# Kernel optimization log

Hardware: AMD Instinct MI355X
Metric: run time of the kernel (lower is better)

The kernel has to match this reference:

```python
import jax, jax.numpy as jnp
import numpy as np

THETA = 10000.0


def rope_apply(x, pos, theta=THETA):
    # x: [..., S, d] with d even; rotates interleaved pairs (2k, 2k+1),
    # matching the block-diag 2x2 rotation matmul in the torch RoPE.
    d = x.shape[-1]
    half = d // 2
    inv_freq = 1.0 / (theta ** (2.0 * jnp.arange(half, dtype=jnp.float32) / d))
    ang = pos.astype(jnp.float32)[:, None] * inv_freq[None, :]  # [S, half]
    cos, sin = jnp.cos(ang), jnp.sin(ang)
    xe, xo = x[..., 0::2], x[..., 1::2]
    oe = cos * xe - sin * xo
    oo = sin * xe + cos * xo
    return jnp.stack([oe, oo], axis=-1).reshape(x.shape)


def setup_inputs() -> dict:
    key = jax.random.key(0)
    ks = jax.random.split(key, 5)
    B, S, D = 2, 2048, 1024
    scale = 0.02
    return {
        "x": jax.random.normal(ks[0], (B, S, D), dtype=jnp.float32),
        "token_positions": jnp.arange(S, dtype=jnp.int64 if jax.config.jax_enable_x64 else jnp.int32),
        "wq": jax.random.normal(ks[1], (D, D), dtype=jnp.float32) * scale,
        "wk": jax.random.normal(ks[2], (D, D), dtype=jnp.float32) * scale,
        "wv": jax.random.normal(ks[3], (D, D), dtype=jnp.float32) * scale,
        "wo": jax.random.normal(ks[4], (D, D), dtype=jnp.float32) * scale,
    }


def reference(x, token_positions, wq, wk, wv, wo):
    B, S, D = x.shape
    H = 16
    dk = D // H

    def split_heads(t):  # [B,S,D] -> [B,H,S,dk]
        return t.reshape(B, S, H, dk).swapaxes(1, 2)

    q = split_heads(jnp.einsum('bsd,ed->bse', x, wq))
    k = split_heads(jnp.einsum('bsd,ed->bse', x, wk))
    v = split_heads(jnp.einsum('bsd,ed->bse', x, wv))

    q = rope_apply(q, token_positions)
    k = rope_apply(k, token_positions)

    scores = jnp.einsum('bhqd,bhkd->bhqk', q, k) / jnp.sqrt(jnp.float32(dk))
    causal = jnp.tril(jnp.ones((S, S), dtype=bool))
    scores = jnp.where(causal, scores, -jnp.inf)
    p = jax.nn.softmax(scores, axis=-1)
    o = jnp.einsum('bhqk,bhkd->bhqd', p, v)          # [B,H,S,dk]
    o = o.swapaxes(1, 2).reshape(B, S, D)            # merge heads
    return jnp.einsum('bse,de->bsd', o, wo)          # out proj (wo.T)
```

## Files before the change

kernel.cpp:

```cpp
#include <hip/hip_runtime.h>

typedef unsigned short u16;
typedef __attribute__((ext_vector_type(8))) short short8;
typedef __attribute__((ext_vector_type(4))) float f32x4;

__device__ __forceinline__ u16 f2b(float f) {
  union { float f; unsigned u; } v; v.f = f;
  unsigned u = v.u;
  return (u16)((u + 0x7FFFu + ((u >> 16) & 1u)) >> 16);
}
__device__ __forceinline__ u16 f2b_trunc(float f) {
  union { float f; unsigned u; } v; v.f = f;
  return (u16)(v.u >> 16);
}
__device__ __forceinline__ void glds16(const u16* g, u16* l) {
  __builtin_amdgcn_global_load_lds((const __attribute__((address_space(1))) void*)g,
                                   (__attribute__((address_space(3))) void*)l, 16, 0, 0);
}

__global__ __launch_bounds__(256) void prep_k(const float* __restrict__ x,
                                              const float* __restrict__ wq,
                                              const float* __restrict__ wk,
                                              const float* __restrict__ wv,
                                              const float* __restrict__ wo,
                                              const int* __restrict__ pos,
                                              u16* __restrict__ xb,
                                              u16* __restrict__ wqkvb,
                                              u16* __restrict__ wob,
                                              float* __restrict__ cs) {
  int bx = blockIdx.x, tid = threadIdx.x;
  if (bx < 8192) {
    const float* src; u16* dst; int base;
    if (bx < 4096)      { src = x;  dst = xb;                base = bx; }
    else if (bx < 5120) { src = wq; dst = wqkvb;             base = bx - 4096; }
    else if (bx < 6144) { src = wk; dst = wqkvb + (1 << 20); base = bx - 5120; }
    else if (bx < 7168) { src = wv; dst = wqkvb + (2 << 20); base = bx - 6144; }
    else                { src = wo; dst = wob;               base = bx - 7168; }
    int i4 = base * 1024 + tid * 4;
    const float4 v = *(const float4*)(src + i4);
    uint2 o;
    o.x = (unsigned)f2b(v.x) | ((unsigned)f2b(v.y) << 16);
    o.y = (unsigned)f2b(v.z) | ((unsigned)f2b(v.w) << 16);
    *(uint2*)(dst + i4) = o;
  } else {
    int idx = (bx - 8192) * 256 + tid;
    int i = idx & 31, s = idx >> 5;
    float p = (float)pos[s];
    float inv = expf(-(float)i * (logf(10000.0f) / 32.0f));
    float ang = p * inv;
    cs[idx * 2]     = cosf(ang);
    cs[idx * 2 + 1] = sinf(ang);
  }
}

__global__ __launch_bounds__(256, 3) void gemm_qkv(const u16* __restrict__ A,
                                                   const u16* __restrict__ B,
                                                   const float* __restrict__ cs,
                                                   u16* __restrict__ Qr,
                                                   u16* __restrict__ Kr,
                                                   u16* __restrict__ VTg) {
  const int K = 1024;
  __shared__ u16 As[128 * 64];
  __shared__ u16 Bs[128 * 64];
  const int tid = threadIdx.x;
  const int lane = tid & 63;
  const int wvid = tid >> 6;
  const int wr = wvid >> 1, wc = wvid & 1;
  const int quad = lane >> 4, l16 = lane & 15;
  const int lin = blockIdx.x + blockIdx.y * 24;
  const int chunk = lin >> 3;
  const int ncol = (lin & 7) * 3 + (chunk % 3);
  const int nrow = chunk / 3;
  const int m0 = nrow * 128, n0 = ncol * 128;
  const int sw = l16 & 7;

  f32x4 acc[4][4];
  for (int i = 0; i < 4; i++)
    for (int j = 0; j < 4; j++) acc[i][j] = (f32x4){0.f, 0.f, 0.f, 0.f};

  for (int kt = 0; kt < K; kt += 64) {
    __syncthreads();
#pragma unroll
    for (int p = 0; p < 4; p++) {
      int c = p * 256 + tid;
      int row = c >> 3, k8 = (c & 7) ^ (row & 7);
      glds16(A + (size_t)(m0 + row) * K + kt + k8 * 8, As + (size_t)(c & ~63) * 8);
    }
#pragma unroll
    for (int p = 0; p < 4; p++) {
      int c = p * 256 + tid;
      int row = c >> 3, k8 = (c & 7) ^ (row & 7);
      glds16(B + (size_t)(n0 + row) * K + kt + k8 * 8, Bs + (size_t)(c & ~63) * 8);
    }
    __syncthreads();
#pragma unroll
    for (int half = 0; half < 2; half++) {
      short8 af[4], bfr[4];
      const int kc = ((half * 4 + quad) ^ sw) * 8;
#pragma unroll
      for (int i = 0; i < 4; i++)
        af[i] = *(const short8*)(As + (wr * 64 + i * 16 + l16) * 64 + kc);
#pragma unroll
      for (int j = 0; j < 4; j++)
        bfr[j] = *(const short8*)(Bs + (wc * 64 + j * 16 + l16) * 64 + kc);
#pragma unroll
      for (int i = 0; i < 4; i++)
#pragma unroll
        for (int j = 0; j < 4; j++)
          acc[i][j] = __builtin_amdgcn_mfma_f32_16x16x32_bf16(af[i], bfr[j], acc[i][j], 0, 0, 0);
    }
  }

  const int region = n0 >> 10;
  const int b = m0 >> 11;
  if (region < 2) {
    u16* dst = region ? Kr : Qr;
    const float qs = region ? 1.0f : 0.125f * 1.44269504f;
    const bool evn = (l16 & 1) == 0;
    for (int i = 0; i < 4; i++)
      for (int j = 0; j < 4; j++) {
        int col = n0 + wc * 64 + j * 16 + l16;
        int cq = col & 1023;
        int h = cq >> 6, d = cq & 63, ifr = (d >> 1) & 31;
        for (int r = 0; r < 4; r++) {
          int s = (m0 & 2047) + wr * 64 + i * 16 + quad * 4 + r;
          float v = acc[i][j][r];
          float vp = __shfl_xor(v, 1);
          if (evn) {
            float2 c2 = *(const float2*)(cs + (s * 32 + ifr) * 2);
            float oe = (c2.x * v - c2.y * vp) * qs;
            float oo = (c2.y * v + c2.x * vp) * qs;
            unsigned pk = (unsigned)f2b(oe) | ((unsigned)f2b(oo) << 16);
            *(unsigned*)(dst + ((size_t)(b * 16 + h) * 2048 + s) * 64 + d) = pk;
          }
        }
      }
  } else {
    for (int j = 0; j < 4; j++) {
      int col = n0 + wc * 64 + j * 16 + l16;
      int cq = col & 1023;
      int h = cq >> 6, d = cq & 63;
      u16* base = VTg + ((size_t)(b * 16 + h) * 64 + d) * 2048;
      for (int i = 0; i < 4; i++) {
        int s0 = (m0 & 2047) + wr * 64 + i * 16 + quad * 4;
        uint2 o;
        o.x = (unsigned)f2b(acc[i][j][0]) | ((unsigned)f2b(acc[i][j][1]) << 16);
        o.y = (unsigned)f2b(acc[i][j][2]) | ((unsigned)f2b(acc[i][j][3]) << 16);
        *(uint2*)(base + s0) = o;
      }
    }
  }
}

__global__ __launch_bounds__(256, 2) void gemm_bt_f32(const u16* __restrict__ A,
                                                      const u16* __restrict__ B,
                                                      float* __restrict__ C,
                                                      int M, int N, int K) {
  __shared__ u16 As[64 * 64];
  __shared__ u16 Bs[128 * 64];
  const int tid = threadIdx.x;
  const int wv = tid >> 6, lane = tid & 63;
  const int quad = lane >> 4, l16 = lane & 15;
  const int m0 = blockIdx.y * 64, n0 = blockIdx.x * 128;
  const int sw = l16 & 7;

  f32x4 acc[4][2];
  for (int i = 0; i < 4; i++)
    for (int j = 0; j < 2; j++) acc[i][j] = (f32x4){0.f, 0.f, 0.f, 0.f};

  for (int kt = 0; kt < K; kt += 64) {
    __syncthreads();
#pragma unroll
    for (int p = 0; p < 2; p++) {
      int c = p * 256 + tid;
      int row = c >> 3, k8 = (c & 7) ^ (row & 7);
      glds16(A + (size_t)(m0 + row) * K + kt + k8 * 8, As + (size_t)(c & ~63) * 8);
    }
#pragma unroll
    for (int p = 0; p < 4; p++) {
      int c = p * 256 + tid;
      int row = c >> 3, k8 = (c & 7) ^ (row & 7);
      glds16(B + (size_t)(n0 + row) * K + kt + k8 * 8, Bs + (size_t)(c & ~63) * 8);
    }
    __syncthreads();
#pragma unroll
    for (int half = 0; half < 2; half++) {
      short8 af[4], bfr[2];
      const int kc = ((half * 4 + quad) ^ sw) * 8;
#pragma unroll
      for (int i = 0; i < 4; i++)
        af[i] = *(const short8*)(As + (i * 16 + l16) * 64 + kc);
#pragma unroll
      for (int j = 0; j < 2; j++)
        bfr[j] = *(const short8*)(Bs + (wv * 32 + j * 16 + l16) * 64 + kc);
#pragma unroll
      for (int i = 0; i < 4; i++)
#pragma unroll
        for (int j = 0; j < 2; j++)
          acc[i][j] = __builtin_amdgcn_mfma_f32_16x16x32_bf16(af[i], bfr[j], acc[i][j], 0, 0, 0);
    }
  }
  for (int i = 0; i < 4; i++)
    for (int j = 0; j < 2; j++) {
      int col = n0 + wv * 32 + j * 16 + l16;
      for (int r = 0; r < 4; r++) {
        int row = m0 + i * 16 + quad * 4 + r;
        C[(size_t)row * N + col] = acc[i][j][r];
      }
    }
}

struct AttnSM {
  u16 Ks[2][8 * 512];
  u16 Vt[2][8 * 512];
  u16 Ps[2][8 * 520];
};

template <bool DIAG>
__device__ __forceinline__ void attn_tile(const u16* Ksb, const u16* Vtb, u16* Psb,
                                          short8 qa0, short8 qa1, f32x4* oacc,
                                          f32x4& lacc, int wl, int quad, int l16) {
  const int rowbase = wl * 16 + quad * 4;
#pragma unroll
  for (int nt = 0; nt < 4; nt++) {
    f32x4 s4 = (f32x4){0.f, 0.f, 0.f, 0.f};
    short8 b0 = *(const short8*)(Ksb + quad * 512 + (nt * 16 + l16) * 8);
    short8 b1 = *(const short8*)(Ksb + (4 + quad) * 512 + (nt * 16 + l16) * 8);
    s4 = __builtin_amdgcn_mfma_f32_16x16x32_bf16(qa0, b0, s4, 0, 0, 0);
    s4 = __builtin_amdgcn_mfma_f32_16x16x32_bf16(qa1, b1, s4, 0, 0, 0);
    int col = nt * 16 + l16;
    int cp = col >> 3, co = col & 7;
#pragma unroll
    for (int r = 0; r < 4; r++) {
      float v = s4[r];
      if (DIAG && col > rowbase + r) v = -1e30f;
      float p = exp2f(v);
      int row = rowbase + r;
      int A = (cp + 2 * (row >> 3)) & 7;
      Psb[A * 520 + row * 8 + co] = f2b_trunc(p);
    }
  }
  int mr = wl * 16 + l16;
  int A0 = (quad + 2 * (mr >> 3)) & 7;
  short8 pa0 = *(const short8*)(Psb + A0 * 520 + mr * 8);
  short8 pa1 = *(const short8*)(Psb + ((A0 + 4) & 7) * 520 + mr * 8);
  const short8 ones = (short8){(short)0x3F80, (short)0x3F80, (short)0x3F80, (short)0x3F80,
                               (short)0x3F80, (short)0x3F80, (short)0x3F80, (short)0x3F80};
  lacc = __builtin_amdgcn_mfma_f32_16x16x32_bf16(pa0, ones, lacc, 0, 0, 0);
  lacc = __builtin_amdgcn_mfma_f32_16x16x32_bf16(pa1, ones, lacc, 0, 0, 0);
  int sl0 = quad ^ (l16 & 7);
#pragma unroll
  for (int nt = 0; nt < 4; nt++) {
    int d = nt * 16 + l16;
    short8 vb0 = *(const short8*)(Vtb + d * 64 + sl0 * 8);
    short8 vb1 = *(const short8*)(Vtb + d * 64 + (sl0 ^ 4) * 8);
    oacc[nt] = __builtin_amdgcn_mfma_f32_16x16x32_bf16(pa0, vb0, oacc[nt], 0, 0, 0);
    oacc[nt] = __builtin_amdgcn_mfma_f32_16x16x32_bf16(pa1, vb1, oacc[nt], 0, 0, 0);
  }
}

__global__ __launch_bounds__(512, 4) void attn_k(const u16* __restrict__ Q,
                                                 const u16* __restrict__ K,
                                                 const u16* __restrict__ VT,
                                                 u16* __restrict__ O, int S) {
  __shared__ AttnSM sm;
  const int tid = threadIdx.x;
  const int wv = tid >> 6, lane = tid & 63, quad = lane >> 4, l16 = lane & 15;
  const int grp = wv >> 2, wl = wv & 3;
  const int bh = blockIdx.x, slot = blockIdx.y;
  const int qtB = 31 - slot;
  const int qtMy = grp ? qtB : slot;
  const int q0My = qtMy * 64;
  const u16* Qg = Q + (size_t)bh * S * 64;
  const u16* Kg = K + (size_t)bh * S * 64;
  const u16* Vg = VT + (size_t)bh * S * 64;
  const int vrow_off = lane >> 3;
  const int vchunk = (lane & 7) ^ (lane >> 3);

  const u16* qrow = Qg + (size_t)(q0My + wl * 16 + l16) * 64;
  short8 qa0 = *(const short8*)(qrow + quad * 8);
  short8 qa1 = *(const short8*)(qrow + 32 + quad * 8);

  f32x4 oacc[4];
  for (int j = 0; j < 4; j++) oacc[j] = (f32x4){0.f, 0.f, 0.f, 0.f};
  f32x4 lacc = (f32x4){0.f, 0.f, 0.f, 0.f};
  u16* Psb = &sm.Ps[grp][0];

  glds16(Kg + (size_t)lane * 64 + wv * 8, &sm.Ks[0][wv * 512]);
  glds16(Vg + (size_t)(wv * 8 + vrow_off) * S + vchunk * 8, &sm.Vt[0][wv * 512]);

  for (int kt = 0; kt <= qtB; kt++) {
    const int cur = kt & 1;
    __syncthreads();
    if (kt < qtB) {
      const int kn = (kt + 1) * 64;
      glds16(Kg + (size_t)(kn + lane) * 64 + wv * 8, &sm.Ks[cur ^ 1][wv * 512]);
      glds16(Vg + (size_t)(wv * 8 + vrow_off) * S + kn + vchunk * 8, &sm.Vt[cur ^ 1][wv * 512]);
    }
    if (kt < qtMy)
      attn_tile<false>(&sm.Ks[cur][0], &sm.Vt[cur][0], Psb, qa0, qa1, oacc, lacc, wl, quad, l16);
    else if (kt == qtMy)
      attn_tile<true>(&sm.Ks[cur][0], &sm.Vt[cur][0], Psb, qa0, qa1, oacc, lacc, wl, quad, l16);
  }

  const int b = bh >> 4, h = bh & 15;
  const bool evn = (l16 & 1) == 0;
  const int rowbase = wl * 16 + quad * 4;
  float l_inv[4];
#pragma unroll
  for (int r = 0; r < 4; r++) l_inv[r] = 1.f / lacc[r];
#pragma unroll
  for (int nt = 0; nt < 4; nt++) {
    int col = nt * 16 + l16;
#pragma unroll
    for (int r = 0; r < 4; r++) {
      float v = oacc[nt][r] * l_inv[r];
      float vp = __shfl_xor(v, 1);
      if (evn) {
        int s = q0My + rowbase + r;
        unsigned pk = (unsigned)f2b(v) | ((unsigned)f2b(vp) << 16);
        *(unsigned*)(O + ((size_t)(b * S + s) * 16 + h) * 64 + col) = pk;
      }
    }
  }
}

extern "C" void kernel_launch(void* const* d_in, const int* in_sizes, int n_in,
                              void* d_out, int out_size, void* d_ws, size_t ws_size,
                              hipStream_t stream) {
  const float* x  = (const float*)d_in[0];
  const int*   tp = (const int*)d_in[1];
  const float* wq = (const float*)d_in[2];
  const float* wk = (const float*)d_in[3];
  const float* wvp = (const float*)d_in[4];
  const float* wo = (const float*)d_in[5];
  float* out = (float*)d_out;

  const int S = 2048, D = 1024;
  const int BS = 2 * S;

  char* ws = (char*)d_ws;
  u16*   xb    = (u16*)(ws);
  u16*   wqkvb = (u16*)(ws + ((size_t)8 << 20));
  u16*   wob   = (u16*)(ws + ((size_t)14 << 20));
  float* cs    = (float*)(ws + ((size_t)16 << 20));
  u16*   qr    = (u16*)(ws + ((size_t)17 << 20));
  u16*   kr    = (u16*)(ws + ((size_t)25 << 20));
  u16*   vtg   = (u16*)(ws + ((size_t)33 << 20));
  u16*   ob    = (u16*)(ws + ((size_t)42 << 20));

  prep_k<<<8448, 256, 0, stream>>>(x, wq, wk, wvp, wo, tp, xb, wqkvb, wob, cs);

  dim3 g1(3 * D / 128, BS / 128);
  gemm_qkv<<<g1, 256, 0, stream>>>(xb, wqkvb, cs, qr, kr, vtg);

  dim3 ga(32, 16);
  attn_k<<<ga, 512, 0, stream>>>(qr, kr, vtg, ob, S);

  dim3 g2(D / 128, BS / 64);
  gemm_bt_f32<<<g2, 256, 0, stream>>>(ob, wob, out, BS, D, D);
}
```

Baseline: 179.0 us.

## Process both paired query tiles per wave to share K/V fragment loads

The attention kernel drops from 512 to 256 threads per block, and each wave now handles rows from both the low and the high query tile of a causal pair. A new fused tile routine reuses each K and V LDS fragment for the two query tiles, where before two wave groups each loaded them separately. It also removes the idle time of the first group, which previously sat out the iterations past its diagonal. In exchange each thread holds twice the accumulators, raising register pressure, and there are fewer waves per block to hide latency.

```diff
diff --git a/kernel.cpp b/kernel.cpp
--- a/kernel.cpp
+++ b/kernel.cpp
@@ -259,35 +259,102 @@
   }
 }
 
-__global__ __launch_bounds__(512, 4) void attn_k(const u16* __restrict__ Q,
+template <bool DIAGA>
+__device__ __forceinline__ void attn_tile2(const u16* Ksb, const u16* Vtb,
+                                           u16* PsA, u16* PsB,
+                                           short8 qaA0, short8 qaA1,
+                                           short8 qaB0, short8 qaB1,
+                                           f32x4* oaccA, f32x4* oaccB,
+                                           f32x4& laccA, f32x4& laccB,
+                                           int wl, int quad, int l16) {
+  const int rowbase = wl * 16 + quad * 4;
+#pragma unroll
+  for (int nt = 0; nt < 4; nt++) {
+    short8 b0 = *(const short8*)(Ksb + quad * 512 + (nt * 16 + l16) * 8);
+    short8 b1 = *(const short8*)(Ksb + (4 + quad) * 512 + (nt * 16 + l16) * 8);
+    f32x4 sA = (f32x4){0.f, 0.f, 0.f, 0.f};
+    f32x4 sB = (f32x4){0.f, 0.f, 0.f, 0.f};
+    sA = __builtin_amdgcn_mfma_f32_16x16x32_bf16(qaA0, b0, sA, 0, 0, 0);
+    sA = __builtin_amdgcn_mfma_f32_16x16x32_bf16(qaA1, b1, sA, 0, 0, 0);
+    sB = __builtin_amdgcn_mfma_f32_16x16x32_bf16(qaB0, b0, sB, 0, 0, 0);
+    sB = __builtin_amdgcn_mfma_f32_16x16x32_bf16(qaB1, b1, sB, 0, 0, 0);
+    int col = nt * 16 + l16;
+    int cp = col >> 3, co = col & 7;
+#pragma unroll
+    for (int r = 0; r < 4; r++) {
+      float vA = sA[r];
+      if (DIAGA && col > rowbase + r) vA = -1e30f;
+      float pA = exp2f(vA);
+      float pB = exp2f(sB[r]);
+      int row = rowbase + r;
+      int A = (cp + 2 * (row >> 3)) & 7;
+      PsA[A * 520 + row * 8 + co] = f2b_trunc(pA);
+      PsB[A * 520 + row * 8 + co] = f2b_trunc(pB);
+    }
+  }
+  int mr = wl * 16 + l16;
+  int A0 = (quad + 2 * (mr >> 3)) & 7;
+  short8 paA0 = *(const short8*)(PsA + A0 * 520 + mr * 8);
+  short8 paA1 = *(const short8*)(PsA + ((A0 + 4) & 7) * 520 + mr * 8);
+  short8 paB0 = *(const short8*)(PsB + A0 * 520 + mr * 8);
+  short8 paB1 = *(const short8*)(PsB + ((A0 + 4) & 7) * 520 + mr * 8);
+  const short8 ones = (short8){(short)0x3F80, (short)0x3F80, (short)0x3F80, (short)0x3F80,
+                               (short)0x3F80, (short)0x3F80, (short)0x3F80, (short)0x3F80};
+  laccA = __builtin_amdgcn_mfma_f32_16x16x32_bf16(paA0, ones, laccA, 0, 0, 0);
+  laccA = __builtin_amdgcn_mfma_f32_16x16x32_bf16(paA1, ones, laccA, 0, 0, 0);
+  laccB = __builtin_amdgcn_mfma_f32_16x16x32_bf16(paB0, ones, laccB, 0, 0, 0);
+  laccB = __builtin_amdgcn_mfma_f32_16x16x32_bf16(paB1, ones, laccB, 0, 0, 0);
+  int sl0 = quad ^ (l16 & 7);
+#pragma unroll
+  for (int nt = 0; nt < 4; nt++) {
+    int d = nt * 16 + l16;
+    short8 vb0 = *(const short8*)(Vtb + d * 64 + sl0 * 8);
+    short8 vb1 = *(const short8*)(Vtb + d * 64 + (sl0 ^ 4) * 8);
+    oaccA[nt] = __builtin_amdgcn_mfma_f32_16x16x32_bf16(paA0, vb0, oaccA[nt], 0, 0, 0);
+    oaccA[nt] = __builtin_amdgcn_mfma_f32_16x16x32_bf16(paA1, vb1, oaccA[nt], 0, 0, 0);
+    oaccB[nt] = __builtin_amdgcn_mfma_f32_16x16x32_bf16(paB0, vb0, oaccB[nt], 0, 0, 0);
+    oaccB[nt] = __builtin_amdgcn_mfma_f32_16x16x32_bf16(paB1, vb1, oaccB[nt], 0, 0, 0);
+  }
+}
+
+__global__ __launch_bounds__(256, 2) void attn_k(const u16* __restrict__ Q,
                                                  const u16* __restrict__ K,
                                                  const u16* __restrict__ VT,
                                                  u16* __restrict__ O, int S) {
   __shared__ AttnSM sm;
   const int tid = threadIdx.x;
   const int wv = tid >> 6, lane = tid & 63, quad = lane >> 4, l16 = lane & 15;
-  const int grp = wv >> 2, wl = wv & 3;
+  const int wl = wv;
   const int bh = blockIdx.x, slot = blockIdx.y;
-  const int qtB = 31 - slot;
-  const int qtMy = grp ? qtB : slot;
-  const int q0My = qtMy * 64;
+  const int qtA = slot, qtB = 31 - slot;
+  const int q0A = qtA * 64, q0B = qtB * 64;
   const u16* Qg = Q + (size_t)bh * S * 64;
   const u16* Kg = K + (size_t)bh * S * 64;
   const u16* Vg = VT + (size_t)bh * S * 64;
   const int vrow_off = lane >> 3;
   const int vchunk = (lane & 7) ^ (lane >> 3);
 
-  const u16* qrow = Qg + (size_t)(q0My + wl * 16 + l16) * 64;
-  short8 qa0 = *(const short8*)(qrow + quad * 8);
-  short8 qa1 = *(const short8*)(qrow + 32 + quad * 8);
-
-  f32x4 oacc[4];
-  for (int j = 0; j < 4; j++) oacc[j] = (f32x4){0.f, 0.f, 0.f, 0.f};
-  f32x4 lacc = (f32x4){0.f, 0.f, 0.f, 0.f};
-  u16* Psb = &sm.Ps[grp][0];
+  const u16* qrowA = Qg + (size_t)(q0A + wl * 16 + l16) * 64;
+  const u16* qrowB = Qg + (size_t)(q0B + wl * 16 + l16) * 64;
+  short8 qaA0 = *(const short8*)(qrowA + quad * 8);
+  short8 qaA1 = *(const short8*)(qrowA + 32 + quad * 8);
+  short8 qaB0 = *(const short8*)(qrowB + quad * 8);
+  short8 qaB1 = *(const short8*)(qrowB + 32 + quad * 8);
+
+  f32x4 oaccA[4], oaccB[4];
+  for (int j = 0; j < 4; j++) {
+    oaccA[j] = (f32x4){0.f, 0.f, 0.f, 0.f};
+    oaccB[j] = (f32x4){0.f, 0.f, 0.f, 0.f};
+  }
+  f32x4 laccA = (f32x4){0.f, 0.f, 0.f, 0.f};
+  f32x4 laccB = (f32x4){0.f, 0.f, 0.f, 0.f};
+  u16* PsA = &sm.Ps[0][0];
+  u16* PsB = &sm.Ps[1][0];
 
   glds16(Kg + (size_t)lane * 64 + wv * 8, &sm.Ks[0][wv * 512]);
+  glds16(Kg + (size_t)lane * 64 + (wv + 4) * 8, &sm.Ks[0][(wv + 4) * 512]);
   glds16(Vg + (size_t)(wv * 8 + vrow_off) * S + vchunk * 8, &sm.Vt[0][wv * 512]);
+  glds16(Vg + (size_t)((wv + 4) * 8 + vrow_off) * S + vchunk * 8, &sm.Vt[0][(wv + 4) * 512]);
 
   for (int kt = 0; kt <= qtB; kt++) {
     const int cur = kt & 1;
@@ -295,31 +362,50 @@
     if (kt < qtB) {
       const int kn = (kt + 1) * 64;
       glds16(Kg + (size_t)(kn + lane) * 64 + wv * 8, &sm.Ks[cur ^ 1][wv * 512]);
+      glds16(Kg + (size_t)(kn + lane) * 64 + (wv + 4) * 8, &sm.Ks[cur ^ 1][(wv + 4) * 512]);
       glds16(Vg + (size_t)(wv * 8 + vrow_off) * S + kn + vchunk * 8, &sm.Vt[cur ^ 1][wv * 512]);
-    }
-    if (kt < qtMy)
-      attn_tile<false>(&sm.Ks[cur][0], &sm.Vt[cur][0], Psb, qa0, qa1, oacc, lacc, wl, quad, l16);
-    else if (kt == qtMy)
-      attn_tile<true>(&sm.Ks[cur][0], &sm.Vt[cur][0], Psb, qa0, qa1, oacc, lacc, wl, quad, l16);
+      glds16(Vg + (size_t)((wv + 4) * 8 + vrow_off) * S + kn + vchunk * 8,
+             &sm.Vt[cur ^ 1][(wv + 4) * 512]);
+    }
+    if (kt < qtA)
+      attn_tile2<false>(&sm.Ks[cur][0], &sm.Vt[cur][0], PsA, PsB,
+                        qaA0, qaA1, qaB0, qaB1, oaccA, oaccB, laccA, laccB, wl, quad, l16);
+    else if (kt == qtA)
+      attn_tile2<true>(&sm.Ks[cur][0], &sm.Vt[cur][0], PsA, PsB,
+                       qaA0, qaA1, qaB0, qaB1, oaccA, oaccB, laccA, laccB, wl, quad, l16);
+    else if (kt < qtB)
+      attn_tile<false>(&sm.Ks[cur][0], &sm.Vt[cur][0], PsB, qaB0, qaB1, oaccB, laccB,
+                       wl, quad, l16);
+    else
+      attn_tile<true>(&sm.Ks[cur][0], &sm.Vt[cur][0], PsB, qaB0, qaB1, oaccB, laccB,
+                      wl, quad, l16);
   }
 
   const int b = bh >> 4, h = bh & 15;
   const bool evn = (l16 & 1) == 0;
   const int rowbase = wl * 16 + quad * 4;
-  float l_inv[4];
-#pragma unroll
-  for (int r = 0; r < 4; r++) l_inv[r] = 1.f / lacc[r];
+  float liA[4], liB[4];
+#pragma unroll
+  for (int r = 0; r < 4; r++) {
+    liA[r] = 1.f / laccA[r];
+    liB[r] = 1.f / laccB[r];
+  }
 #pragma unroll
   for (int nt = 0; nt < 4; nt++) {
     int col = nt * 16 + l16;
 #pragma unroll
     for (int r = 0; r < 4; r++) {
-      float v = oacc[nt][r] * l_inv[r];
-      float vp = __shfl_xor(v, 1);
+      float vA = oaccA[nt][r] * liA[r];
+      float vpA = __shfl_xor(vA, 1);
+      float vB = oaccB[nt][r] * liB[r];
+      float vpB = __shfl_xor(vB, 1);
       if (evn) {
-        int s = q0My + rowbase + r;
-        unsigned pk = (unsigned)f2b(v) | ((unsigned)f2b(vp) << 16);
-        *(unsigned*)(O + ((size_t)(b * S + s) * 16 + h) * 64 + col) = pk;
+        int sA = q0A + rowbase + r;
+        unsigned pkA = (unsigned)f2b(vA) | ((unsigned)f2b(vpA) << 16);
+        *(unsigned*)(O + ((size_t)(b * S + sA) * 16 + h) * 64 + col) = pkA;
+        int sB = q0B + rowbase + r;
+        unsigned pkB = (unsigned)f2b(vB) | ((unsigned)f2b(vpB) << 16);
+        *(unsigned*)(O + ((size_t)(b * S + sB) * 16 + h) * 64 + col) = pkB;
       }
     }
   }
@@ -355,7 +441,7 @@
   gemm_qkv<<<g1, 256, 0, stream>>>(xb, wqkvb, cs, qr, kr, vtg);
 
   dim3 ga(32, 16);
-  attn_k<<<ga, 512, 0, stream>>>(qr, kr, vtg, ob, S);
+  attn_k<<<ga, 256, 0, stream>>>(qr, kr, vtg, ob, S);
 
   dim3 g2(D / 128, BS / 64);
   gemm_bt_f32<<<g2, 256, 0, stream>>>(ob, wob, out, BS, D, D);
```

Measured after the change: 193.1 us. 7.9% more time.
